# Performance work log

Measured on AMD Instinct MI355X. Metric: run time of the kernel, lower is better.

The kernel has to match this reference:

```python
import jax, jax.numpy as jnp
import numpy as np

LOG2 = float(np.log(2.0))

def _ssp(x):
    # shifted softplus: ln(0.5*(exp(x)+1)) = softplus(x) - ln 2
    return jax.nn.softplus(x) - LOG2

def setup_inputs() -> dict:
    key = jax.random.key(0)
    ks = jax.random.split(key, 8)
    B, N, D = 32, 512, 1024
    H = D // 2
    s = lambda fan_in: 1.0 / np.sqrt(fan_in)
    return {
        "representation": jax.random.normal(ks[0], (B, N, D), jnp.float32),
        "R": jax.random.normal(ks[1], (B, N, 3), jnp.float32),
        "atom_mask": jnp.ones((B, N), jnp.float32),
        "W1": jax.random.normal(ks[2], (D, H), jnp.float32) * s(D),
        "b1": jnp.zeros((H,), jnp.float32),
        "W2": jax.random.normal(ks[3], (H, 1), jnp.float32) * s(H),
        "b2": jnp.zeros((1,), jnp.float32),
        "Wc1": jax.random.normal(ks[4], (D, H), jnp.float32) * s(D),
        "bc1": jnp.zeros((H,), jnp.float32),
        "Wc2": jax.random.normal(ks[5], (H, 1), jnp.float32) * s(H),
        "bc2": jnp.zeros((1,), jnp.float32),
    }

def reference(representation, R, atom_mask, W1, b1, W2, b2, Wc1, bc1, Wc2, bc2):
    B, N, _ = representation.shape
    # Atomwise pyramidal MLP: n_in -> n_in//2 (shifted softplus) -> 1
    yi = _ssp(jnp.einsum("bnd,dh->bnh", representation, W1) + b1)
    yi = jnp.einsum("bnh,ho->bno", yi, W2) + b2            # [B,N,1]
    # masked sum pool over atoms (mean=0, stddev=1 so standardize is identity)
    y = jnp.sum(yi * atom_mask[..., None], axis=1)          # [B,1]

    # pairwise distances with safe sqrt (diag is exactly zero)
    diff = R[:, None, :, :] - R[:, :, None, :]              # [B,N,N,3]
    d2 = jnp.sum(diff * diff, axis=-1)                      # [B,N,N]
    dist = jnp.where(d2 > 0, jnp.sqrt(jnp.where(d2 > 0, d2, 1.0)), 0.0)

    eye = jnp.eye(N, dtype=dist.dtype)
    tot_mask = atom_mask[:, None, :] * atom_mask[:, :, None] * (1.0 - eye)
    keep = (tot_mask != 0).astype(dist.dtype)               # [B,N,N]
    dist = dist * keep

    # charge net: Dense(n_in, n_in//2, ssp) -> Dense(n_in//2, 1)
    q = _ssp(jnp.einsum("bnd,dh->bnh", representation, Wc1) + bc1)
    q = jnp.einsum("bnh,ho->bno", q, Wc2) + bc2             # [B,N,1]

    inv2 = (1e-5 + dist) ** -2                              # [B,N,N]
    coulomb = q[:, :, 0][:, None, :] * inv2 * q             # [B,N,N] (q_j * inv * q_i)
    coulomb = coulomb * keep
    e = jnp.sum(coulomb, axis=(1, 2))                       # [B]

    return y + e[:, None]                                   # [B,1]
```

## Files before the change

kernel.cpp:

```cpp
#include <hip/hip_runtime.h>
#include <math.h>


typedef unsigned short u16;
typedef unsigned int u32;
typedef __bf16 bf16x8 __attribute__((ext_vector_type(8)));
typedef float f32x4 __attribute__((ext_vector_type(4)));

#define GK 1024

#define GLOAD_LDS16(g, l) __builtin_amdgcn_global_load_lds( \
    (const __attribute__((address_space(1))) void*)(g),     \
    (__attribute__((address_space(3))) void*)(l), 16, 0, 0)

__device__ __forceinline__ u16 f2bf(float f) {
    u32 u = __float_as_uint(f);
    return (u16)((u + 0x7FFFu + ((u >> 16) & 1u)) >> 16);
}

__device__ __forceinline__ float ssp_f(float x) {
    return __logf(0.5f * (__expf(x) + 1.0f));
}

__device__ __forceinline__ float ssp_slow(float x) {
    return fmaxf(x, 0.0f) + log1pf(expf(-fabsf(x))) - 0.6931471805599453f;
}


__global__ __launch_bounds__(256) void prep(
    const float* __restrict__ rep, const float* __restrict__ W1,
    const float* __restrict__ Wc1, u16* __restrict__ Abf,
    u16* __restrict__ Btb, float* __restrict__ out)
{
    __shared__ float tile[32][33];
    const int blk = blockIdx.x;
    const int t = threadIdx.x;
    if (blk < 8192) {
        int i = (blk * 256 + t) * 8;
        float4 x = *(const float4*)(rep + i);
        float4 y = *(const float4*)(rep + i + 4);
        union { u16 h[8]; uint4 v; } o;
        o.h[0] = f2bf(x.x); o.h[1] = f2bf(x.y); o.h[2] = f2bf(x.z); o.h[3] = f2bf(x.w);
        o.h[4] = f2bf(y.x); o.h[5] = f2bf(y.y); o.h[6] = f2bf(y.z); o.h[7] = f2bf(y.w);
        *(uint4*)(Abf + i) = o.v;
        if (blk == 0 && t < 32) out[t] = 0.0f;
    } else {
        const int bb = blk - 8192;
        const int k0 = (bb & 31) * 32;
        const int n0 = (bb >> 5) * 32;
        const float* src = (n0 < 512) ? W1 : Wc1;
        const int ns0 = (n0 < 512) ? n0 : n0 - 512;
#pragma unroll
        for (int j = 0; j < 4; j++) {
            int idx = j * 256 + t;
            int kl = idx >> 5, nl = idx & 31;
            tile[kl][nl] = src[(size_t)(k0 + kl) * 512 + ns0 + nl];
        }
        __syncthreads();
#pragma unroll
        for (int j = 0; j < 4; j++) {
            int idx = j * 256 + t;
            int nl = idx >> 5, kl = idx & 31;
            Btb[(size_t)(n0 + nl) * 1024 + k0 + kl] = f2bf(tile[kl][nl]);
        }
    }
}


__global__ __launch_bounds__(512) void gemm_mfma(
    const u16* __restrict__ A,
    const u16* __restrict__ Bt,
    const float* __restrict__ b1, const float* __restrict__ W2,
    const float* __restrict__ bc1, const float* __restrict__ Wc2,
    float* __restrict__ parts)
{
    __shared__ u16 As[256 * 32];
    __shared__ u16 Bs[128 * 32];
    __shared__ float red[2][256];
    const int blk = blockIdx.x;
    const int bm = ((blk & 7) << 3) | (blk >> 6);
    const int bn = (blk >> 3) & 7;
    const int tid = threadIdx.x;
    const int w = tid >> 6, lane = tid & 63;
    const int wave_m = w & 3, wave_n = w >> 2;
    const int lm = lane & 15, q = lane >> 4;

    f32x4 acc[4][4];
#pragma unroll
    for (int i = 0; i < 4; i++)
#pragma unroll
        for (int j = 0; j < 4; j++)
            acc[i][j] = (f32x4){0.0f, 0.0f, 0.0f, 0.0f};

    int gaoff[2];
#pragma unroll
    for (int p = 0; p < 2; p++) {
        int c = (w * 2 + p) * 64 + lane;
        int line = c >> 3, sp = c & 7;
        int un = sp ^ (line & 7);
        int row = line + 128 * (un >> 2);
        int k8 = un & 3;
        gaoff[p] = row * GK + k8 * 8;
    }
    int gboff;
    {
        int c = w * 64 + lane;
        int line = c >> 3, sp = c & 7;
        int un = sp ^ (line & 7);
        int row = ((un >> 2) << 6) | line;
        int k8 = un & 3;
        gboff = row * GK + k8 * 8;
    }

    int aoff[4], boff[4];
#pragma unroll
    for (int i = 0; i < 4; i++) {
        int mrow = wave_m * 64 + i * 16 + lm;
        int la = mrow & 127;
        aoff[i] = la * 64 + ((((mrow >> 7) << 2) | q) ^ (la & 7)) * 8;
        int nrow = wave_n * 64 + i * 16 + lm;
        int lb = nrow & 63;
        boff[i] = lb * 64 + ((((nrow >> 6) << 2) | q) ^ (lb & 7)) * 8;
    }

    const u16* Ab = A + (size_t)(bm * 256) * GK;
    const u16* Bb = Bt + (size_t)(bn * 128) * GK;

    for (int kt = 0; kt < GK; kt += 32) {
#pragma unroll
        for (int p = 0; p < 2; p++)
            GLOAD_LDS16(Ab + kt + gaoff[p], &As[(w * 2 + p) << 9]);
        GLOAD_LDS16(Bb + kt + gboff, &Bs[w << 9]);
        __syncthreads();
        bf16x8 af[4], bfr[4];
#pragma unroll
        for (int i = 0; i < 4; i++) {
            af[i] = *(const bf16x8*)&As[aoff[i]];
            bfr[i] = *(const bf16x8*)&Bs[boff[i]];
        }
#pragma unroll
        for (int i = 0; i < 4; i++)
#pragma unroll
            for (int j = 0; j < 4; j++)
                acc[i][j] = __builtin_amdgcn_mfma_f32_16x16x32_bf16(
                    af[i], bfr[j], acc[i][j], 0, 0, 0);
        __syncthreads();
    }

    const bool is_q = (bn >= 4);
    const float* bb2 = is_q ? bc1 : b1;
    const float* vv = is_q ? Wc2 : W2;
    const int cb0 = (bn & 3) * 128 + wave_n * 64;
    float bias[4], v[4];
#pragma unroll
    for (int j = 0; j < 4; j++) {
        int c = cb0 + j * 16 + lm;
        bias[j] = bb2[c];
        v[j] = vv[c];
    }
#pragma unroll
    for (int i = 0; i < 4; i++) {
#pragma unroll
        for (int r = 0; r < 4; r++) {
            float s = 0.0f;
#pragma unroll
            for (int j = 0; j < 4; j++)
                s += v[j] * ssp_f(acc[i][j][r] + bias[j]);
            s += __shfl_xor(s, 1);
            s += __shfl_xor(s, 2);
            s += __shfl_xor(s, 4);
            s += __shfl_xor(s, 8);
            if (lm == 0) red[wave_n][wave_m * 64 + i * 16 + q * 4 + r] = s;
        }
    }
    __syncthreads();
    if (tid < 256) {
        float val = red[0][tid] + red[1][tid];
        parts[(size_t)((is_q ? 4 : 0) + (bn & 3)) * 16384 + bm * 256 + tid] = val;
    }
}


__global__ __launch_bounds__(256) void coulomb_k(
    const float* __restrict__ R, const float* __restrict__ mask,
    const float* __restrict__ parts, const float* __restrict__ b2p,
    const float* __restrict__ bc2p, float* __restrict__ out)
{
    const int N = 512;
    const int b = blockIdx.y;
    const int chunk = blockIdx.x;
    __shared__ float Rx[512], Ry[512], Rz[512], QM[512];
    __shared__ float rbuf[4];
    const int tid = threadIdx.x;
    const float bc2 = bc2p[0];
    const float b2 = b2p[0];

    for (int j = tid; j < N; j += 256) {
        int idx = b * N + j;
        float m = mask[idx];
        const float* rp = R + (size_t)idx * 3;
        Rx[j] = rp[0];
        Ry[j] = rp[1];
        Rz[j] = rp[2];
        float qv = parts[4 * 16384 + idx] + parts[5 * 16384 + idx] +
                   parts[6 * 16384 + idx] + parts[7 * 16384 + idx] + bc2;
        QM[j] = qv * m;
    }
    __syncthreads();

    const int i = chunk * 64 + (tid & 63);
    const int js = (tid >> 6) * 128;
    const float xi = Rx[i], yi = Ry[i], zi = Rz[i], qmi = QM[i];
    float e = 0.0f;
    for (int j = js; j < js + 128; j++) {
        float dx = xi - Rx[j];
        float dy = yi - Ry[j];
        float dz = zi - Rz[j];
        float d2 = dx * dx + dy * dy + dz * dz;
        float t = 1e-5f + sqrtf(d2);
        float term = qmi * QM[j] / (t * t);
        e += (j == i) ? 0.0f : term;
    }
    if (tid < 64) {
        int ii = b * N + chunk * 64 + tid;
        float yv = parts[0 * 16384 + ii] + parts[1 * 16384 + ii] +
                   parts[2 * 16384 + ii] + parts[3 * 16384 + ii] + b2;
        e += yv * mask[ii];
    }
    for (int off = 32; off > 0; off >>= 1) e += __shfl_down(e, off, 64);
    if ((tid & 63) == 0) rbuf[tid >> 6] = e;
    __syncthreads();
    if (tid == 0) atomicAdd(&out[b], rbuf[0] + rbuf[1] + rbuf[2] + rbuf[3]);
}


#define BM 128
#define BN 64
#define BK 16

__global__ __launch_bounds__(256) void mlp_gemm(
    const float* __restrict__ A, const float* __restrict__ W1,
    const float* __restrict__ Wc1, const float* __restrict__ b1,
    const float* __restrict__ bc1, const float* __restrict__ W2,
    const float* __restrict__ Wc2, float* __restrict__ yi_part,
    float* __restrict__ q_part)
{
    const int K = 1024;
    const int bm = blockIdx.x;
    const int bn = blockIdx.y;
    const bool is_q = (bn >= 8);
    const float* __restrict__ W = is_q ? Wc1 : W1;
    const int j0 = (bn & 7) * BN;

    __shared__ float As[BK][BM + 4];
    __shared__ float Bs[BK][BN + 4];
    __shared__ float red[BM];

    const int tid = threadIdx.x;
    const int tx = tid & 15;
    const int ty = tid >> 4;

    float acc[8][4];
#pragma unroll
    for (int r = 0; r < 8; r++)
#pragma unroll
        for (int c = 0; c < 4; c++) acc[r][c] = 0.0f;

    const int a_row = tid >> 2;
    const int a_k4 = (tid & 3) * 4;
    const float* Arow0 = A + (size_t)(bm * BM + a_row) * K;
    const float* Arow1 = Arow0 + (size_t)64 * K;
    const int w_k = tid >> 4;
    const int w_j = (tid & 15) * 4;

    for (int kt = 0; kt < K; kt += BK) {
        float4 av0 = *(const float4*)(Arow0 + kt + a_k4);
        float4 av1 = *(const float4*)(Arow1 + kt + a_k4);
        float4 wv = *(const float4*)(W + (size_t)(kt + w_k) * 512 + j0 + w_j);
        __syncthreads();
        As[a_k4 + 0][a_row] = av0.x;
        As[a_k4 + 1][a_row] = av0.y;
        As[a_k4 + 2][a_row] = av0.z;
        As[a_k4 + 3][a_row] = av0.w;
        As[a_k4 + 0][a_row + 64] = av1.x;
        As[a_k4 + 1][a_row + 64] = av1.y;
        As[a_k4 + 2][a_row + 64] = av1.z;
        As[a_k4 + 3][a_row + 64] = av1.w;
        *(float4*)&Bs[w_k][w_j] = wv;
        __syncthreads();
#pragma unroll
        for (int kk = 0; kk < BK; kk++) {
            float4 a0 = *(const float4*)&As[kk][ty * 8];
            float4 a1 = *(const float4*)&As[kk][ty * 8 + 4];
            float4 bv = *(const float4*)&Bs[kk][tx * 4];
            float ar[8] = {a0.x, a0.y, a0.z, a0.w, a1.x, a1.y, a1.z, a1.w};
            float bc[4] = {bv.x, bv.y, bv.z, bv.w};
#pragma unroll
            for (int r = 0; r < 8; r++)
#pragma unroll
                for (int c = 0; c < 4; c++)
                    acc[r][c] = fmaf(ar[r], bc[c], acc[r][c]);
        }
    }

    const float* bb = is_q ? bc1 : b1;
    const float* vv = is_q ? Wc2 : W2;
    float bias[4], v[4];
#pragma unroll
    for (int c = 0; c < 4; c++) {
        bias[c] = bb[j0 + tx * 4 + c];
        v[c] = vv[j0 + tx * 4 + c];
    }
    if (tid < BM) red[tid] = 0.0f;
    __syncthreads();
#pragma unroll
    for (int r = 0; r < 8; r++) {
        float s = 0.0f;
#pragma unroll
        for (int c = 0; c < 4; c++)
            s += v[c] * ssp_slow(acc[r][c] + bias[c]);
        atomicAdd(&red[ty * 8 + r], s);
    }
    __syncthreads();
    float* target = is_q ? q_part : yi_part;
    if (tid < BM) atomicAdd(&target[(size_t)bm * BM + tid], red[tid]);
}

__global__ __launch_bounds__(256) void coulomb_fb(
    const float* __restrict__ R, const float* __restrict__ mask,
    const float* __restrict__ yi_part, const float* __restrict__ q_part,
    const float* __restrict__ b2p, const float* __restrict__ bc2p,
    float* __restrict__ out)
{
    const int N = 512;
    const int b = blockIdx.y;
    const int chunk = blockIdx.x;
    __shared__ float Rx[512], Ry[512], Rz[512], QM[512];
    __shared__ float rbuf[4];
    const int tid = threadIdx.x;
    const float bc2 = bc2p[0];
    const float b2 = b2p[0];

    for (int j = tid; j < N; j += 256) {
        float m = mask[b * N + j];
        const float* rp = R + ((size_t)b * N + j) * 3;
        Rx[j] = rp[0];
        Ry[j] = rp[1];
        Rz[j] = rp[2];
        QM[j] = (q_part[b * N + j] + bc2) * m;
    }
    __syncthreads();

    const int i = chunk * 64 + (tid & 63);
    const int js = (tid >> 6) * 128;
    const float xi = Rx[i], yi = Ry[i], zi = Rz[i], qmi = QM[i];
    float e = 0.0f;
    for (int j = js; j < js + 128; j++) {
        float dx = xi - Rx[j];
        float dy = yi - Ry[j];
        float dz = zi - Rz[j];
        float d2 = dx * dx + dy * dy + dz * dz;
        float t = 1e-5f + sqrtf(d2);
        float term = qmi * QM[j] / (t * t);
        e += (j == i) ? 0.0f : term;
    }
    if (tid < 64) {
        int ii = chunk * 64 + tid;
        e += (yi_part[b * N + ii] + b2) * mask[b * N + ii];
    }
    for (int off = 32; off > 0; off >>= 1) e += __shfl_down(e, off, 64);
    if ((tid & 63) == 0) rbuf[tid >> 6] = e;
    __syncthreads();
    if (tid == 0) atomicAdd(&out[b], rbuf[0] + rbuf[1] + rbuf[2] + rbuf[3]);
}


extern "C" void kernel_launch(void* const* d_in, const int* in_sizes, int n_in,
                              void* d_out, int out_size, void* d_ws, size_t ws_size,
                              hipStream_t stream) {
    const float* rep  = (const float*)d_in[0];
    const float* R    = (const float*)d_in[1];
    const float* mask = (const float*)d_in[2];
    const float* W1   = (const float*)d_in[3];
    const float* b1   = (const float*)d_in[4];
    const float* W2   = (const float*)d_in[5];
    const float* b2   = (const float*)d_in[6];
    const float* Wc1  = (const float*)d_in[7];
    const float* bc1  = (const float*)d_in[8];
    const float* Wc2  = (const float*)d_in[9];
    const float* bc2  = (const float*)d_in[10];
    float* out = (float*)d_out;

    const size_t szA = 16384ull * 1024 * 2;
    const size_t szB = 1024ull * 1024 * 2;
    const size_t szP = 8ull * 16384 * 4;
    const size_t need = szA + szB + szP;

    if (ws_size >= need) {
        u16* Abf = (u16*)d_ws;
        u16* Btb = (u16*)((char*)d_ws + szA);
        float* parts = (float*)((char*)d_ws + szA + szB);

        prep<<<8192 + 1024, 256, 0, stream>>>(rep, W1, Wc1, Abf, Btb, out);
        gemm_mfma<<<512, 512, 0, stream>>>(Abf, Btb, b1, W2, bc1, Wc2, parts);
        coulomb_k<<<dim3(8, 32), 256, 0, stream>>>(R, mask, parts, b2, bc2, out);
    } else {
        float* yi_part = (float*)d_ws;
        float* q_part = yi_part + 16384;
        hipMemsetAsync(d_ws, 0, 2 * 16384 * sizeof(float), stream);
        hipMemsetAsync(d_out, 0, 32 * sizeof(float), stream);
        mlp_gemm<<<dim3(128, 16), 256, 0, stream>>>(rep, W1, Wc1, b1, bc1, W2, Wc2,
                                                    yi_part, q_part);
        coulomb_fb<<<dim3(8, 32), 256, 0, stream>>>(R, mask, yi_part, q_part, b2, bc2, out);
    }
}
```

Measured before the change: 171.8 us.

## Use 256x256 double-buffered MFMA tiles with phased LDS staging in GEMM

The bf16 MFMA GEMM now computes 256x256 output tiles per block (256 blocks instead of 512) with a K-step of 64 and double-buffered LDS. Global-to-LDS loads for the next K-tile are issued in halves between four MFMA quadrants, with s_setprio raised around the MFMA bursts. The larger tile cuts global and LDS traffic per flop and hides load latency behind compute. In exchange each wave holds twice as many accumulators, which raises register pressure, and the 256-block grid may leave some compute units with uneven work. The partial-sum layout shrinks from 8 to 4 slices, and the Coulomb kernel reads it accordingly.

Result: no change. 169.7 us (-1.2%).

```diff
diff --git a/kernel.cpp b/kernel.cpp
--- a/kernel.cpp
+++ b/kernel.cpp
@@ -8,6 +8,7 @@
 typedef float f32x4 __attribute__((ext_vector_type(4)));
 
 #define GK 1024
+#define NT 16
 
 #define GLOAD_LDS16(g, l) __builtin_amdgcn_global_load_lds( \
     (const __attribute__((address_space(1))) void*)(g),     \
@@ -67,116 +68,163 @@
 }
 
 
-__global__ __launch_bounds__(512) void gemm_mfma(
+__global__ __launch_bounds__(512, 2) void gemm_mfma(
     const u16* __restrict__ A,
     const u16* __restrict__ Bt,
     const float* __restrict__ b1, const float* __restrict__ W2,
     const float* __restrict__ bc1, const float* __restrict__ Wc2,
     float* __restrict__ parts)
 {
-    __shared__ u16 As[256 * 32];
-    __shared__ u16 Bs[128 * 32];
-    __shared__ float red[2][256];
+    __shared__ u16 smem[2][32768];
+
     const int blk = blockIdx.x;
-    const int bm = ((blk & 7) << 3) | (blk >> 6);
-    const int bn = (blk >> 3) & 7;
+    const int swz = ((blk & 7) << 5) | (blk >> 3);
+    const int bm = swz >> 2;
+    const int bn = swz & 3;
     const int tid = threadIdx.x;
     const int w = tid >> 6, lane = tid & 63;
-    const int wave_m = w & 3, wave_n = w >> 2;
+    const int wm = w & 1, wn = w >> 1;
     const int lm = lane & 15, q = lane >> 4;
 
-    f32x4 acc[4][4];
-#pragma unroll
-    for (int i = 0; i < 4; i++)
+    f32x4 acc[8][4];
+#pragma unroll
+    for (int i = 0; i < 8; i++)
 #pragma unroll
         for (int j = 0; j < 4; j++)
             acc[i][j] = (f32x4){0.0f, 0.0f, 0.0f, 0.0f};
 
-    int gaoff[2];
-#pragma unroll
-    for (int p = 0; p < 2; p++) {
-        int c = (w * 2 + p) * 64 + lane;
-        int line = c >> 3, sp = c & 7;
-        int un = sp ^ (line & 7);
-        int row = line + 128 * (un >> 2);
-        int k8 = un & 3;
-        gaoff[p] = row * GK + k8 * 8;
-    }
-    int gboff;
+    int goff[2][2];
+#pragma unroll
+    for (int h = 0; h < 2; h++)
+#pragma unroll
+        for (int p2 = 0; p2 < 2; p2++) {
+            int ci = h * 1024 + (w * 2 + p2) * 64 + lane;
+            int row = ci >> 3;
+            int c = (ci & 7) ^ (row & 7);
+            goff[h][p2] = row * GK + c * 8;
+        }
+
+    int arow[4], brow[2], aswz[2];
+#pragma unroll
+    for (int mi = 0; mi < 4; mi++) arow[mi] = (wm * 128 + mi * 16 + lm) * 64;
+#pragma unroll
+    for (int nj = 0; nj < 2; nj++) brow[nj] = (wn * 64 + nj * 16 + lm) * 64;
+#pragma unroll
+    for (int kk = 0; kk < 2; kk++) aswz[kk] = ((kk * 4 + q) ^ (lm & 7)) * 8;
+
+    const u16* Ab = A + (size_t)bm * 256 * GK;
+    const u16* Bb = Bt + (size_t)bn * 256 * GK;
+
+#define STAGE_HT(G, RG, H) do {                                               \
+    GLOAD_LDS16((G) + goff[H][0], &smem[nxt][(RG) + ((H) * 1024 + (w * 2 + 0) * 64) * 8]); \
+    GLOAD_LDS16((G) + goff[H][1], &smem[nxt][(RG) + ((H) * 1024 + (w * 2 + 1) * 64) * 8]); \
+} while (0)
+
+#define READ_A(MH)                                                            \
+    _Pragma("unroll") for (int mi = 0; mi < 4; mi++)                          \
+    _Pragma("unroll") for (int kk = 0; kk < 2; kk++)                          \
+        afr[mi][kk] = *(const bf16x8*)&smem[cur][arow[mi] + (MH) * 4096 + aswz[kk]];
+
+#define READ_B(NH)                                                            \
+    _Pragma("unroll") for (int nj = 0; nj < 2; nj++)                          \
+    _Pragma("unroll") for (int kk = 0; kk < 2; kk++)                          \
+        bfr2[nj][kk] = *(const bf16x8*)&smem[cur][16384 + brow[nj] + (NH) * 2048 + aswz[kk]];
+
+#define MFMA_QUAD(MH, NH)                                                     \
+    _Pragma("unroll") for (int kk = 0; kk < 2; kk++)                          \
+    _Pragma("unroll") for (int mi = 0; mi < 4; mi++)                          \
+    _Pragma("unroll") for (int nj = 0; nj < 2; nj++)                          \
+        acc[(MH) * 4 + mi][(NH) * 2 + nj] = __builtin_amdgcn_mfma_f32_16x16x32_bf16( \
+            afr[mi][kk], bfr2[nj][kk], acc[(MH) * 4 + mi][(NH) * 2 + nj], 0, 0, 0);
+
     {
-        int c = w * 64 + lane;
-        int line = c >> 3, sp = c & 7;
-        int un = sp ^ (line & 7);
-        int row = ((un >> 2) << 6) | line;
-        int k8 = un & 3;
-        gboff = row * GK + k8 * 8;
-    }
-
-    int aoff[4], boff[4];
-#pragma unroll
-    for (int i = 0; i < 4; i++) {
-        int mrow = wave_m * 64 + i * 16 + lm;
-        int la = mrow & 127;
-        aoff[i] = la * 64 + ((((mrow >> 7) << 2) | q) ^ (la & 7)) * 8;
-        int nrow = wave_n * 64 + i * 16 + lm;
-        int lb = nrow & 63;
-        boff[i] = lb * 64 + ((((nrow >> 6) << 2) | q) ^ (lb & 7)) * 8;
-    }
-
-    const u16* Ab = A + (size_t)(bm * 256) * GK;
-    const u16* Bb = Bt + (size_t)(bn * 128) * GK;
-
-    for (int kt = 0; kt < GK; kt += 32) {
-#pragma unroll
-        for (int p = 0; p < 2; p++)
-            GLOAD_LDS16(Ab + kt + gaoff[p], &As[(w * 2 + p) << 9]);
-        GLOAD_LDS16(Bb + kt + gboff, &Bs[w << 9]);
-        __syncthreads();
-        bf16x8 af[4], bfr[4];
-#pragma unroll
-        for (int i = 0; i < 4; i++) {
-            af[i] = *(const bf16x8*)&As[aoff[i]];
-            bfr[i] = *(const bf16x8*)&Bs[boff[i]];
-        }
-#pragma unroll
-        for (int i = 0; i < 4; i++)
-#pragma unroll
-            for (int j = 0; j < 4; j++)
-                acc[i][j] = __builtin_amdgcn_mfma_f32_16x16x32_bf16(
-                    af[i], bfr[j], acc[i][j], 0, 0, 0);
-        __syncthreads();
-    }
-
-    const bool is_q = (bn >= 4);
+        const int nxt = 0;
+#pragma unroll
+        for (int h = 0; h < 2; h++) {
+            STAGE_HT(Ab, 0, h);
+            STAGE_HT(Bb, 16384, h);
+        }
+    }
+    asm volatile("s_waitcnt vmcnt(0)" ::: "memory");
+    __builtin_amdgcn_s_barrier();
+
+    bf16x8 afr[4][2], bfr2[2][2];
+
+    for (int t = 0; t < NT; ++t) {
+        const int cur = t & 1, nxt = cur ^ 1;
+        const bool st = (t < NT - 1);
+        const u16* gA = Ab + ((t + 1) & (NT - 1)) * 64;
+        const u16* gB = Bb + ((t + 1) & (NT - 1)) * 64;
+
+        if (st) { STAGE_HT(gA, 0, 0); STAGE_HT(gB, 16384, 0); }
+        READ_A(0); READ_B(0);
+        __builtin_amdgcn_s_barrier();
+        __builtin_amdgcn_s_setprio(1);
+        MFMA_QUAD(0, 0);
+        __builtin_amdgcn_s_setprio(0);
+        __builtin_amdgcn_s_barrier();
+
+        if (st) { STAGE_HT(gA, 0, 1); STAGE_HT(gB, 16384, 1); }
+        READ_B(1);
+        __builtin_amdgcn_s_barrier();
+        __builtin_amdgcn_s_setprio(1);
+        MFMA_QUAD(0, 1);
+        __builtin_amdgcn_s_setprio(0);
+        __builtin_amdgcn_s_barrier();
+
+        READ_A(1);
+        __builtin_amdgcn_s_barrier();
+        __builtin_amdgcn_s_setprio(1);
+        MFMA_QUAD(1, 1);
+        __builtin_amdgcn_s_setprio(0);
+        __builtin_amdgcn_s_barrier();
+
+        READ_B(0);
+        __builtin_amdgcn_s_barrier();
+        __builtin_amdgcn_s_setprio(1);
+        MFMA_QUAD(1, 0);
+        __builtin_amdgcn_s_setprio(0);
+        if (st) asm volatile("s_waitcnt vmcnt(0)" ::: "memory");
+        __builtin_amdgcn_s_barrier();
+    }
+
+#undef STAGE_HT
+#undef READ_A
+#undef READ_B
+#undef MFMA_QUAD
+
+    __syncthreads();
+    float* red = (float*)&smem[0][0];
+    const bool is_q = (bn >= 2);
     const float* bb2 = is_q ? bc1 : b1;
     const float* vv = is_q ? Wc2 : W2;
-    const int cb0 = (bn & 3) * 128 + wave_n * 64;
     float bias[4], v[4];
 #pragma unroll
-    for (int j = 0; j < 4; j++) {
-        int c = cb0 + j * 16 + lm;
-        bias[j] = bb2[c];
-        v[j] = vv[c];
-    }
-#pragma unroll
-    for (int i = 0; i < 4; i++) {
+    for (int nfr = 0; nfr < 4; nfr++) {
+        int c = (bn & 1) * 256 + wn * 64 + nfr * 16 + lm;
+        bias[nfr] = bb2[c];
+        v[nfr] = vv[c];
+    }
+#pragma unroll
+    for (int mfr = 0; mfr < 8; mfr++) {
 #pragma unroll
         for (int r = 0; r < 4; r++) {
             float s = 0.0f;
 #pragma unroll
-            for (int j = 0; j < 4; j++)
-                s += v[j] * ssp_f(acc[i][j][r] + bias[j]);
+            for (int nfr = 0; nfr < 4; nfr++)
+                s += v[nfr] * ssp_f(acc[mfr][nfr][r] + bias[nfr]);
             s += __shfl_xor(s, 1);
             s += __shfl_xor(s, 2);
             s += __shfl_xor(s, 4);
             s += __shfl_xor(s, 8);
-            if (lm == 0) red[wave_n][wave_m * 64 + i * 16 + q * 4 + r] = s;
+            if (lm == 0) red[wn * 256 + wm * 128 + mfr * 16 + q * 4 + r] = s;
         }
     }
     __syncthreads();
     if (tid < 256) {
-        float val = red[0][tid] + red[1][tid];
-        parts[(size_t)((is_q ? 4 : 0) + (bn & 3)) * 16384 + bm * 256 + tid] = val;
+        float val = red[0 * 256 + tid] + red[1 * 256 + tid] +
+                    red[2 * 256 + tid] + red[3 * 256 + tid];
+        parts[(size_t)bn * 16384 + bm * 256 + tid] = val;
     }
 }
 
@@ -202,8 +250,7 @@
         Rx[j] = rp[0];
         Ry[j] = rp[1];
         Rz[j] = rp[2];
-        float qv = parts[4 * 16384 + idx] + parts[5 * 16384 + idx] +
-                   parts[6 * 16384 + idx] + parts[7 * 16384 + idx] + bc2;
+        float qv = parts[2 * 16384 + idx] + parts[3 * 16384 + idx] + bc2;
         QM[j] = qv * m;
     }
     __syncthreads();
@@ -223,8 +270,7 @@
     }
     if (tid < 64) {
         int ii = b * N + chunk * 64 + tid;
-        float yv = parts[0 * 16384 + ii] + parts[1 * 16384 + ii] +
-                   parts[2 * 16384 + ii] + parts[3 * 16384 + ii] + b2;
+        float yv = parts[0 * 16384 + ii] + parts[1 * 16384 + ii] + b2;
         e += yv * mask[ii];
     }
     for (int off = 32; off > 0; off >>= 1) e += __shfl_down(e, off, 64);
@@ -402,7 +448,7 @@
         float* parts = (float*)((char*)d_ws + szA + szB);
 
         prep<<<8192 + 1024, 256, 0, stream>>>(rep, W1, Wc1, Abf, Btb, out);
-        gemm_mfma<<<512, 512, 0, stream>>>(Abf, Btb, b1, W2, bc1, Wc2, parts);
+        gemm_mfma<<<256, 512, 0, stream>>>(Abf, Btb, b1, W2, bc1, Wc2, parts);
         coulomb_k<<<dim3(8, 32), 256, 0, stream>>>(R, mask, parts, b2, bc2, out);
     } else {
         float* yi_part = (float*)d_ws;
```
